# Kernel optimization log

Measured on AMD Instinct MI355X. Metric: run time of the kernel, lower is better.

## Reference

```python
import jax, jax.numpy as jnp
import numpy as np

D_MODEL = 1024
NUM_HEADS = 16
MAX_LEN = 500
D_K = D_MODEL // NUM_HEADS


def setup_inputs() -> dict:
    key = jax.random.key(0)
    ks = jax.random.split(key, 10)
    B, L = 8, 500
    s = 1.0 / np.sqrt(D_MODEL)
    return {
        "query": jax.random.normal(ks[0], (B, L, D_MODEL), dtype=jnp.float32),
        "key": jax.random.normal(ks[1], (B, L, D_MODEL), dtype=jnp.float32),
        "value": jax.random.normal(ks[2], (B, L, D_MODEL), dtype=jnp.float32),
        "Wq": jax.random.normal(ks[3], (D_MODEL, D_MODEL), dtype=jnp.float32) * s,
        "bq": jnp.zeros((D_MODEL,), dtype=jnp.float32),
        "Wk": jax.random.normal(ks[4], (D_MODEL, D_MODEL), dtype=jnp.float32) * s,
        "bk": jnp.zeros((D_MODEL,), dtype=jnp.float32),
        "Wv": jax.random.normal(ks[5], (D_MODEL, D_MODEL), dtype=jnp.float32) * s,
        "bv": jnp.zeros((D_MODEL,), dtype=jnp.float32),
        "rel_emb": jax.random.normal(ks[6], (NUM_HEADS, 2 * MAX_LEN - 1), dtype=jnp.float32),
    }


def reference(query, key, value, Wq, bq, Wk, bk, Wv, bv, rel_emb):
    B, Lq, _ = query.shape
    Lk = key.shape[1]
    H, dk = NUM_HEADS, D_K
    # QKV projections -> [B, H, L, d]
    q = (query @ Wq + bq).reshape(B, Lq, H, dk).transpose(0, 2, 1, 3)
    k = (key @ Wk + bk).reshape(B, Lk, H, dk).transpose(0, 2, 1, 3)
    v = (value @ Wv + bv).reshape(B, Lk, H, dk).transpose(0, 2, 1, 3)
    scores = jnp.einsum('bhqd,bhkd->bhqk', q, k) / jnp.sqrt(jnp.float32(dk))
    # gathered relative-position bias: [H, Lq, Lk]
    rel_idx = jnp.arange(Lq)[:, None] - jnp.arange(Lk)[None, :] + MAX_LEN - 1
    bias = rel_emb[:, rel_idx]  # [H, Lq, Lk]
    scores = scores + bias[None]
    attn = jax.nn.softmax(scores, axis=-1)
    out = jnp.einsum('bhqk,bhkd->bhqd', attn, v)
    return out.transpose(0, 2, 1, 3).reshape(B, Lq, H * dk)
```

## Files before the change

### kernel.cpp

```cpp
#include <hip/hip_runtime.h>

typedef short bf16x8 __attribute__((ext_vector_type(8)));
typedef float f32x4 __attribute__((ext_vector_type(4)));
typedef unsigned uint4v __attribute__((ext_vector_type(4)));

#define B_    8
#define L_    500
#define LP    512
#define H_    16
#define DK    64
#define DM    1024
#define MP    4096
#define NT    8

static __device__ __forceinline__ unsigned short f2bf(float x) {
  unsigned u = __float_as_uint(x);
  u += 0x7fffu + ((u >> 16) & 1u);
  return (unsigned short)(u >> 16);
}

static __device__ __forceinline__ unsigned cvtpk(float lo, float hi) {
  unsigned r;
  asm("v_cvt_pk_bf16_f32 %0, %1, %2" : "=v"(r) : "v"(lo), "v"(hi));
  return r;
}

static __device__ __forceinline__ void gload16(const void* g, void* l) {
  __builtin_amdgcn_global_load_lds(
      (const __attribute__((address_space(1))) void*)g,
      (__attribute__((address_space(3))) void*)l, 16, 0, 0);
}

__global__ __launch_bounds__(256) void conv_x_kernel(
    const float* __restrict__ iq, const float* __restrict__ ik,
    const float* __restrict__ iv, unsigned short* __restrict__ X) {
  const int z = blockIdx.y;
  const float* src = (z == 0) ? iq : (z == 1) ? ik : iv;
  const size_t flat = (size_t)blockIdx.x * 256 + threadIdx.x;
  const size_t off = flat * 8;
  const int m = (int)(off >> 10);
  unsigned short o[8];
  if (m < 4000) {
    const float4 a = *(const float4*)(src + off);
    const float4 b = *(const float4*)(src + off + 4);
    o[0]=f2bf(a.x); o[1]=f2bf(a.y); o[2]=f2bf(a.z); o[3]=f2bf(a.w);
    o[4]=f2bf(b.x); o[5]=f2bf(b.y); o[6]=f2bf(b.z); o[7]=f2bf(b.w);
  } else {
#pragma unroll
    for (int i = 0; i < 8; ++i) o[i] = 0;
  }
  uint4 pk;
  pk.x = (unsigned)o[0] | ((unsigned)o[1] << 16);
  pk.y = (unsigned)o[2] | ((unsigned)o[3] << 16);
  pk.z = (unsigned)o[4] | ((unsigned)o[5] << 16);
  pk.w = (unsigned)o[6] | ((unsigned)o[7] << 16);
  *(uint4*)(X + (size_t)z * MP * DM + off) = pk;
}

__global__ __launch_bounds__(256) void conv_w_kernel(
    const float* __restrict__ wq, const float* __restrict__ wk,
    const float* __restrict__ wv, unsigned short* __restrict__ Wt) {
  const int z = blockIdx.y;
  const float* W = (z == 0) ? wq : (z == 1) ? wk : wv;
  const int k0 = (blockIdx.x >> 4) * 64;
  const int n0 = (blockIdx.x & 15) * 64;
  __shared__ float t[64][65];
  const int tid = threadIdx.x;
  const int row = tid >> 2;
  const int cb  = (tid & 3) * 16;
#pragma unroll
  for (int s = 0; s < 4; ++s) {
    const float4 v = *(const float4*)(W + (size_t)(k0 + row) * DM + n0 + cb + s * 4);
    t[row][cb + s * 4 + 0] = v.x; t[row][cb + s * 4 + 1] = v.y;
    t[row][cb + s * 4 + 2] = v.z; t[row][cb + s * 4 + 3] = v.w;
  }
  __syncthreads();
  const int nr = tid >> 2;
  const int kb = (tid & 3) * 16;
#pragma unroll
  for (int s = 0; s < 2; ++s) {
    unsigned short o[8];
#pragma unroll
    for (int e = 0; e < 8; ++e) o[e] = f2bf(t[kb + s * 8 + e][nr]);
    uint4 pk;
    pk.x = (unsigned)o[0] | ((unsigned)o[1] << 16);
    pk.y = (unsigned)o[2] | ((unsigned)o[3] << 16);
    pk.z = (unsigned)o[4] | ((unsigned)o[5] << 16);
    pk.w = (unsigned)o[6] | ((unsigned)o[7] << 16);
    *(uint4*)(Wt + (size_t)z * DM * DM + (size_t)(n0 + nr) * DM + k0 + kb + s * 8) = pk;
  }
}

__global__ __launch_bounds__(256) void gemm_qkv_kernel(
    const unsigned short* __restrict__ X, const unsigned short* __restrict__ Wt,
    const float* __restrict__ bq, const float* __restrict__ bk,
    const float* __restrict__ bv,
    unsigned short* __restrict__ qo, unsigned short* __restrict__ ko,
    unsigned short* __restrict__ vo) {
  const int z = blockIdx.y;
  const unsigned short* A  = X  + (size_t)z * MP * DM;
  const unsigned short* Bw = Wt + (size_t)z * DM * DM;
  const float* bias = (z == 0) ? bq : (z == 1) ? bk : bv;
  unsigned short* out = (z == 0) ? qo : (z == 1) ? ko : vo;

  const int bid = blockIdx.x;
  const int xg = bid & 7, y = bid >> 3;
  const int tm = xg + 8 * (y >> 3);
  const int tn = y & 7;
  const int tid = threadIdx.x;
  const int lane = tid & 63, wid = tid >> 6;
  const int wr = wid >> 1, wc = wid & 1;
  const int lg = lane >> 4, lr = lane & 15;

  __shared__ unsigned short sA[2][128 * 32];
  __shared__ unsigned short sB[2][128 * 32];

  const int c0 = tid, c1 = tid + 256;
  const int ar0 = c0 >> 2, ak0 = (c0 & 3) * 8;
  const int ar1 = c1 >> 2, ak1 = (c1 & 3) * 8;
  const unsigned short* Ab = A  + (size_t)tm * 128 * DM;
  const unsigned short* Bb = Bw + (size_t)tn * 128 * DM;

  f32x4 acc[4][4];
#pragma unroll
  for (int i = 0; i < 4; ++i)
#pragma unroll
    for (int j = 0; j < 4; ++j) acc[i][j] = (f32x4){0.f, 0.f, 0.f, 0.f};

  gload16(Ab + (size_t)ar0 * DM + ak0, &sA[0][c0 * 8]);
  gload16(Ab + (size_t)ar1 * DM + ak1, &sA[0][c1 * 8]);
  gload16(Bb + (size_t)ar0 * DM + ak0, &sB[0][c0 * 8]);
  gload16(Bb + (size_t)ar1 * DM + ak1, &sB[0][c1 * 8]);
  asm volatile("s_waitcnt vmcnt(0)" ::: "memory");
  __syncthreads();

  int cur = 0;
  for (int t = 0; t < 32; ++t) {
    if (t < 31) {
      const int kn = (t + 1) * 32;
      gload16(Ab + (size_t)ar0 * DM + kn + ak0, &sA[cur ^ 1][c0 * 8]);
      gload16(Ab + (size_t)ar1 * DM + kn + ak1, &sA[cur ^ 1][c1 * 8]);
      gload16(Bb + (size_t)ar0 * DM + kn + ak0, &sB[cur ^ 1][c0 * 8]);
      gload16(Bb + (size_t)ar1 * DM + kn + ak1, &sB[cur ^ 1][c1 * 8]);
    }
    bf16x8 af[4], bfr[4];
#pragma unroll
    for (int s = 0; s < 4; ++s) {
      af[s]  = *(const bf16x8*)&sA[cur][(wr * 64 + s * 16 + lr) * 32 + lg * 8];
      bfr[s] = *(const bf16x8*)&sB[cur][(wc * 64 + s * 16 + lr) * 32 + lg * 8];
    }
#pragma unroll
    for (int i = 0; i < 4; ++i)
#pragma unroll
      for (int j = 0; j < 4; ++j)
        acc[i][j] = __builtin_amdgcn_mfma_f32_16x16x32_bf16(af[i], bfr[j], acc[i][j], 0, 0, 0);
    asm volatile("s_waitcnt vmcnt(0)" ::: "memory");
    __syncthreads();
    cur ^= 1;
  }

  const int nbase = tn * 128 + wc * 64 + lr;
  float bias4[4];
#pragma unroll
  for (int ns = 0; ns < 4; ++ns) bias4[ns] = bias[nbase + ns * 16];

#pragma unroll
  for (int ms = 0; ms < 4; ++ms) {
#pragma unroll
    for (int r = 0; r < 4; ++r) {
      const int m = tm * 128 + wr * 64 + ms * 16 + lg * 4 + r;
      if (m < 4000) {
        const unsigned batch = (unsigned)m / 500u;
        const int lrow = m - (int)batch * 500;
#pragma unroll
        for (int ns = 0; ns < 4; ++ns) {
          const int n = nbase + ns * 16;
          const int hh = n >> 6, d = n & 63;
          out[(((size_t)batch * H_ + hh) * LP + lrow) * DK + d] =
              f2bf(acc[ms][ns][r] + bias4[ns]);
        }
      }
    }
  }
}

__global__ __launch_bounds__(256) void transpose_v_kernel(
    const unsigned short* __restrict__ v, unsigned short* __restrict__ vt) {
  const int bh = blockIdx.y;
  const int l0 = blockIdx.x * 64;
  __shared__ unsigned short t[64][72];
  const int tid = threadIdx.x;
  const int lrw = tid >> 2, dc = (tid & 3) * 16;
  const int gl = l0 + lrw;
  if (gl < L_) {
    *(uint4*)&t[lrw][dc]     = *(const uint4*)(v + ((size_t)bh * LP + gl) * DK + dc);
    *(uint4*)&t[lrw][dc + 8] = *(const uint4*)(v + ((size_t)bh * LP + gl) * DK + dc + 8);
  } else {
    const uint4 zz = {0u, 0u, 0u, 0u};
    *(uint4*)&t[lrw][dc]     = zz;
    *(uint4*)&t[lrw][dc + 8] = zz;
  }
  __syncthreads();
  const int dr = tid >> 2, lcb = (tid & 3) * 16;
#pragma unroll
  for (int s = 0; s < 2; ++s) {
    unsigned short e[8];
#pragma unroll
    for (int i = 0; i < 8; ++i) e[i] = t[lcb + s * 8 + i][dr];
    uint4 o;
    o.x = (unsigned)e[0] | ((unsigned)e[1] << 16);
    o.y = (unsigned)e[2] | ((unsigned)e[3] << 16);
    o.z = (unsigned)e[4] | ((unsigned)e[5] << 16);
    o.w = (unsigned)e[6] | ((unsigned)e[7] << 16);
    *(uint4*)(vt + ((size_t)bh * DK + dr) * LP + l0 + lcb + s * 8) = o;
  }
}

__global__ __launch_bounds__(256, 4) void attn_kernel(
    const unsigned short* __restrict__ q, const unsigned short* __restrict__ k,
    const unsigned short* __restrict__ vt, const float* __restrict__ rel,
    float* __restrict__ out) {
  const int id = blockIdx.x;
  const int bh = id & 127, qc = id >> 7;
  const int b = bh >> 4, h = bh & 15;
  const int tid = threadIdx.x;
  const int lane = tid & 63, wid = tid >> 6;
  const int lg = lane >> 4, lr = lane & 15;

  __shared__ unsigned short kt[2][2][64][32];
  __shared__ unsigned short vtt[2][2][64][32];
  __shared__ float relb[576];

  const float LOG2E = 1.44269504f;
  const float SC = 0.125f * LOG2E;
  const int rbase = qc * 64 - 12;
  for (int i = tid; i < 575; i += 256) {
    int idx = rbase + i;
    idx = idx < 0 ? 0 : (idx > 998 ? 998 : idx);
    relb[i] = rel[h * 999 + idx] * LOG2E;
  }

  const int qrow = qc * 64 + wid * 16 + lr;
  const unsigned short* qp = q + ((size_t)bh * LP + qrow) * DK + lg * 8;
  const bf16x8 qf0 = *(const bf16x8*)qp;
  const bf16x8 qf1 = *(const bf16x8*)(qp + 32);

  const int kj = tid >> 2, dc = (tid & 3) * 16;
  const unsigned short* kgp = k + ((size_t)bh * LP + kj) * DK + dc;
  unsigned short* kls = &kt[0][dc >> 5][kj][dc & 31];
  const int vd = tid >> 2, vkg = (tid & 3) * 16;
  const unsigned short* vgp = vt + ((size_t)bh * DK + vd) * LP + vkg;
  unsigned short* vls = &vtt[0][vkg >> 5][vd][vkg & 31];

  const int sig0 = 8 * (lr >> 2) + (lr & 3);
  const int qin = wid * 16 + lr;

  f32x4 o[4];
#pragma unroll
  for (int d = 0; d < 4; ++d) o[d] = (f32x4){0.f, 0.f, 0.f, 0.f};
  float mrun = -1e30f, lrun = 0.f;

  uint4 ka0 = *(const uint4*)(kgp);
  uint4 ka1 = *(const uint4*)(kgp + 8);
  uint4 va0 = *(const uint4*)(vgp);
  uint4 va1 = *(const uint4*)(vgp + 8);

  for (int t = 0; t < NT; ++t) {
    const int buf = t & 1;
    *(uint4*)(kls + buf * 4096)     = ka0;
    *(uint4*)(kls + buf * 4096 + 8) = ka1;
    *(uint4*)(vls + buf * 4096)     = va0;
    *(uint4*)(vls + buf * 4096 + 8) = va1;
    __syncthreads();

    if (t < NT - 1) {
      const size_t ko_ = (size_t)(t + 1) * 64 * DK;
      ka0 = *(const uint4*)(kgp + ko_);
      ka1 = *(const uint4*)(kgp + ko_ + 8);
      va0 = *(const uint4*)(vgp + (t + 1) * 64);
      va1 = *(const uint4*)(vgp + (t + 1) * 64 + 8);
    }

    f32x4 s[2][2];
#pragma unroll
    for (int kc = 0; kc < 2; ++kc)
#pragma unroll
      for (int hf = 0; hf < 2; ++hf) {
        const int sg = kc * 32 + hf * 4 + sig0;
        const bf16x8 a0 = *(const bf16x8*)&kt[buf][0][sg][lg * 8];
        const bf16x8 a1 = *(const bf16x8*)&kt[buf][1][sg][lg * 8];
        f32x4 ss = (f32x4){0.f, 0.f, 0.f, 0.f};
        ss = __builtin_amdgcn_mfma_f32_16x16x32_bf16(a0, qf0, ss, 0, 0, 0);
        ss = __builtin_amdgcn_mfma_f32_16x16x32_bf16(a1, qf1, ss, 0, 0, 0);
        s[kc][hf] = ss;
      }

    float sc[2][2][4];
#pragma unroll
    for (int kc = 0; kc < 2; ++kc)
#pragma unroll
      for (int hf = 0; hf < 2; ++hf) {
        const int bidx = qin - (t * 64 + kc * 32 + 8 * lg + 4 * hf) + 511;
#pragma unroll
        for (int r = 0; r < 4; ++r)
          sc[kc][hf][r] = s[kc][hf][r] * SC + relb[bidx - r];
      }
    if (t == NT - 1) {
#pragma unroll
      for (int hf = 0; hf < 2; ++hf)
#pragma unroll
        for (int r = 0; r < 4; ++r)
          if (8 * lg + 4 * hf + r >= 20) sc[1][hf][r] = -1e30f;
    }

    float m0 = fmaxf(fmaxf(sc[0][0][0], sc[0][0][1]), fmaxf(sc[0][0][2], sc[0][0][3]));
    float m1 = fmaxf(fmaxf(sc[0][1][0], sc[0][1][1]), fmaxf(sc[0][1][2], sc[0][1][3]));
    float m2 = fmaxf(fmaxf(sc[1][0][0], sc[1][0][1]), fmaxf(sc[1][0][2], sc[1][0][3]));
    float m3 = fmaxf(fmaxf(sc[1][1][0], sc[1][1][1]), fmaxf(sc[1][1][2], sc[1][1][3]));
    const float mloc = fmaxf(fmaxf(m0, m1), fmaxf(m2, m3));
    if (!__all(mloc - mrun <= 11.5f)) {
      float mx = fmaxf(mloc, mrun);
      mx = fmaxf(mx, __shfl_xor(mx, 16));
      mx = fmaxf(mx, __shfl_xor(mx, 32));
      const float alpha = exp2f(mrun - mx);
      mrun = mx;
      lrun *= alpha;
#pragma unroll
      for (int d = 0; d < 4; ++d) {
        o[d][0] *= alpha; o[d][1] *= alpha; o[d][2] *= alpha; o[d][3] *= alpha;
      }
    }

    float rs = 0.f;
    unsigned pw[2][4];
#pragma unroll
    for (int kc = 0; kc < 2; ++kc)
#pragma unroll
      for (int hf = 0; hf < 2; ++hf) {
        float p0 = exp2f(sc[kc][hf][0] - mrun);
        float p1 = exp2f(sc[kc][hf][1] - mrun);
        float p2 = exp2f(sc[kc][hf][2] - mrun);
        float p3 = exp2f(sc[kc][hf][3] - mrun);
        rs += (p0 + p1) + (p2 + p3);
        pw[kc][hf * 2 + 0] = cvtpk(p0, p1);
        pw[kc][hf * 2 + 1] = cvtpk(p2, p3);
      }
    rs += __shfl_xor(rs, 16);
    rs += __shfl_xor(rs, 32);
    lrun += rs;

#pragma unroll
    for (int kc = 0; kc < 2; ++kc) {
      union { uint4v u; bf16x8 v; } cv;
      cv.u = (uint4v){pw[kc][0], pw[kc][1], pw[kc][2], pw[kc][3]};
      const bf16x8 pf = cv.v;
#pragma unroll
      for (int db = 0; db < 4; ++db) {
        const bf16x8 vf = *(const bf16x8*)&vtt[buf][kc][db * 16 + lr][lg * 8];
        o[db] = __builtin_amdgcn_mfma_f32_16x16x32_bf16(vf, pf, o[db], 0, 0, 0);
      }
    }
  }

  if (qrow < L_) {
    const float inv = 1.0f / lrun;
    float* op = out + ((size_t)b * L_ + qrow) * DM + h * DK + lg * 4;
#pragma unroll
    for (int db = 0; db < 4; ++db) {
      float4 v;
      v.x = o[db][0] * inv; v.y = o[db][1] * inv;
      v.z = o[db][2] * inv; v.w = o[db][3] * inv;
      *(float4*)(op + db * 16) = v;
    }
  }
}

extern "C" void kernel_launch(void* const* d_in, const int* in_sizes, int n_in,
                              void* d_out, int out_size, void* d_ws, size_t ws_size,
                              hipStream_t stream) {
  const float* iq  = (const float*)d_in[0];
  const float* ik  = (const float*)d_in[1];
  const float* iv  = (const float*)d_in[2];
  const float* wq  = (const float*)d_in[3];
  const float* bq  = (const float*)d_in[4];
  const float* wk  = (const float*)d_in[5];
  const float* bk  = (const float*)d_in[6];
  const float* wv  = (const float*)d_in[7];
  const float* bv  = (const float*)d_in[8];
  const float* rel = (const float*)d_in[9];
  float* out = (float*)d_out;

  char* w = (char*)d_ws;
  unsigned short* X   = (unsigned short*)(w);
  unsigned short* Wt  = (unsigned short*)(w + 25165824);
  unsigned short* qb  = (unsigned short*)(w + 31457280);
  unsigned short* kb  = (unsigned short*)(w + 39845888);
  unsigned short* vb  = (unsigned short*)(w + 48234496);
  unsigned short* vtb = (unsigned short*)(w);

  conv_x_kernel<<<dim3(2048, 3), 256, 0, stream>>>(iq, ik, iv, X);
  conv_w_kernel<<<dim3(256, 3), 256, 0, stream>>>(wq, wk, wv, Wt);
  gemm_qkv_kernel<<<dim3(256, 3), 256, 0, stream>>>(X, Wt, bq, bk, bv, qb, kb, vb);
  transpose_v_kernel<<<dim3(8, 128), 256, 0, stream>>>(vb, vtb);
  attn_kernel<<<1024, 256, 0, stream>>>(qb, kb, vtb, rel, out);
}
```

Measured before the change: 90.91 us.

## Restructure QKV GEMM into 256x256 tiles with ping-pong pipelined MFMA schedule

The QKV projection GEMM moves from 128x128 tiles with 256 threads and BK=32 to 256x256 tiles with 512 threads (8 waves) and BK=64. LDS uses an XOR swizzle, and staging is split into quarter-steps interleaved with MFMA clusters under s_setprio and barriers. Block-to-XCD mapping is remapped for L2 locality. The aim is higher arithmetic intensity and better overlap of loads with MFMA, at the cost of only 192 blocks on a 256-CU GPU, which leaves many CUs idle, plus heavy register and LDS use.

After: 85.16 us. 1.07x faster.

```diff
diff --git a/kernel.cpp b/kernel.cpp
--- a/kernel.cpp
+++ b/kernel.cpp
@@ -29,6 +29,10 @@
   __builtin_amdgcn_global_load_lds(
       (const __attribute__((address_space(1))) void*)g,
       (__attribute__((address_space(3))) void*)l, 16, 0, 0);
+}
+
+static __device__ __forceinline__ f32x4 MF(bf16x8 a, bf16x8 b, f32x4 c) {
+  return __builtin_amdgcn_mfma_f32_16x16x32_bf16(a, b, c, 0, 0, 0);
 }
 
 __global__ __launch_bounds__(256) void conv_x_kernel(
@@ -91,93 +95,148 @@
   }
 }
 
-__global__ __launch_bounds__(256) void gemm_qkv_kernel(
+#define BAR()   __builtin_amdgcn_s_barrier()
+#define LGKM0() do { asm volatile("s_waitcnt lgkmcnt(0)" ::: "memory"); \
+                     __builtin_amdgcn_sched_barrier(0); } while (0)
+#define VM0()   asm volatile("s_waitcnt vmcnt(0)" ::: "memory")
+#define PRIO1() __builtin_amdgcn_s_setprio(1)
+#define PRIO0() __builtin_amdgcn_s_setprio(0)
+
+#define HALF_STEP(BK_, KTS_, DOST_)                                              \
+  {                                                                              \
+                      \
+    _Pragma("unroll") for (int mi = 0; mi < 4; ++mi) {                           \
+      aF[mi][0] = rdA(BK_, mi, 0); aF[mi][1] = rdA(BK_, mi, 1); }                \
+    _Pragma("unroll") for (int ni = 0; ni < 2; ++ni) {                           \
+      bF[ni][0] = rdB(BK_, ni, 0); bF[ni][1] = rdB(BK_, ni, 1); }                \
+    if (DOST_) { STAGE((&sA[1 - (BK_)][0][0]), GA0, KTS_);                       \
+                 STAGE((&sA[1 - (BK_)][1][0]), GA1, KTS_); }                     \
+    BAR(); LGKM0(); PRIO1();                                                     \
+    _Pragma("unroll") for (int mi = 0; mi < 4; ++mi)                             \
+      _Pragma("unroll") for (int ni = 0; ni < 2; ++ni) {                         \
+        acc[mi][ni] = MF(aF[mi][0], bF[ni][0], acc[mi][ni]);                     \
+        acc[mi][ni] = MF(aF[mi][1], bF[ni][1], acc[mi][ni]); }                   \
+    PRIO0(); BAR();                                                              \
+                                            \
+    _Pragma("unroll") for (int ni = 0; ni < 2; ++ni) {                           \
+      bF2[ni][0] = rdB(BK_, 2 + ni, 0); bF2[ni][1] = rdB(BK_, 2 + ni, 1); }      \
+    if (DOST_) { STAGE((&sB[1 - (BK_)][0][0]), GB0, KTS_); }                     \
+    BAR(); LGKM0(); PRIO1();                                                     \
+    _Pragma("unroll") for (int mi = 0; mi < 4; ++mi)                             \
+      _Pragma("unroll") for (int ni = 0; ni < 2; ++ni) {                         \
+        acc[mi][2 + ni] = MF(aF[mi][0], bF2[ni][0], acc[mi][2 + ni]);            \
+        acc[mi][2 + ni] = MF(aF[mi][1], bF2[ni][1], acc[mi][2 + ni]); }          \
+    PRIO0(); BAR();                                                              \
+                                            \
+    _Pragma("unroll") for (int mi = 0; mi < 4; ++mi) {                           \
+      aF[mi][0] = rdA(BK_, 4 + mi, 0); aF[mi][1] = rdA(BK_, 4 + mi, 1); }        \
+    if (DOST_) { STAGE((&sB[1 - (BK_)][1][0]), GB1, KTS_); }                     \
+    BAR(); LGKM0(); PRIO1();                                                     \
+    _Pragma("unroll") for (int mi = 0; mi < 4; ++mi)                             \
+      _Pragma("unroll") for (int ni = 0; ni < 2; ++ni) {                         \
+        acc[4 + mi][2 + ni] = MF(aF[mi][0], bF2[ni][0], acc[4 + mi][2 + ni]);    \
+        acc[4 + mi][2 + ni] = MF(aF[mi][1], bF2[ni][1], acc[4 + mi][2 + ni]); }  \
+    PRIO0(); BAR();                                                              \
+                 \
+    _Pragma("unroll") for (int ni = 0; ni < 2; ++ni) {                           \
+      bF[ni][0] = rdB(BK_, ni, 0); bF[ni][1] = rdB(BK_, ni, 1); }                \
+    VM0();                                                                       \
+    BAR(); LGKM0(); PRIO1();                                                     \
+    _Pragma("unroll") for (int mi = 0; mi < 4; ++mi)                             \
+      _Pragma("unroll") for (int ni = 0; ni < 2; ++ni) {                         \
+        acc[4 + mi][ni] = MF(aF[mi][0], bF[ni][0], acc[4 + mi][ni]);             \
+        acc[4 + mi][ni] = MF(aF[mi][1], bF[ni][1], acc[4 + mi][ni]); }           \
+    PRIO0(); BAR();                                                              \
+  }
+
+__global__ __launch_bounds__(512, 2) void gemm_qkv_kernel(
     const unsigned short* __restrict__ X, const unsigned short* __restrict__ Wt,
     const float* __restrict__ bq, const float* __restrict__ bk,
     const float* __restrict__ bv,
     unsigned short* __restrict__ qo, unsigned short* __restrict__ ko,
     unsigned short* __restrict__ vo) {
-  const int z = blockIdx.y;
+  const int bid = blockIdx.x;
+  const int z = bid >> 6, r = bid & 63;
+  const int xcd = r & 7, j = r >> 3;
+  const int tm = (xcd & 3) * 4 + (j & 3);
+  const int tn = (xcd >> 2) * 2 + (j >> 2);
   const unsigned short* A  = X  + (size_t)z * MP * DM;
   const unsigned short* Bw = Wt + (size_t)z * DM * DM;
   const float* bias = (z == 0) ? bq : (z == 1) ? bk : bv;
   unsigned short* out = (z == 0) ? qo : (z == 1) ? ko : vo;
 
-  const int bid = blockIdx.x;
-  const int xg = bid & 7, y = bid >> 3;
-  const int tm = xg + 8 * (y >> 3);
-  const int tn = y & 7;
   const int tid = threadIdx.x;
   const int lane = tid & 63, wid = tid >> 6;
-  const int wr = wid >> 1, wc = wid & 1;
+  const int wr = wid >> 2, wcol = wid & 3;
   const int lg = lane >> 4, lr = lane & 15;
 
-  __shared__ unsigned short sA[2][128 * 32];
-  __shared__ unsigned short sB[2][128 * 32];
-
-  const int c0 = tid, c1 = tid + 256;
-  const int ar0 = c0 >> 2, ak0 = (c0 & 3) * 8;
-  const int ar1 = c1 >> 2, ak1 = (c1 & 3) * 8;
-  const unsigned short* Ab = A  + (size_t)tm * 128 * DM;
-  const unsigned short* Bb = Bw + (size_t)tn * 128 * DM;
-
-  f32x4 acc[4][4];
-#pragma unroll
-  for (int i = 0; i < 4; ++i)
-#pragma unroll
-    for (int j = 0; j < 4; ++j) acc[i][j] = (f32x4){0.f, 0.f, 0.f, 0.f};
-
-  gload16(Ab + (size_t)ar0 * DM + ak0, &sA[0][c0 * 8]);
-  gload16(Ab + (size_t)ar1 * DM + ak1, &sA[0][c1 * 8]);
-  gload16(Bb + (size_t)ar0 * DM + ak0, &sB[0][c0 * 8]);
-  gload16(Bb + (size_t)ar1 * DM + ak1, &sB[0][c1 * 8]);
-  asm volatile("s_waitcnt vmcnt(0)" ::: "memory");
-  __syncthreads();
-
-  int cur = 0;
-  for (int t = 0; t < 32; ++t) {
-    if (t < 31) {
-      const int kn = (t + 1) * 32;
-      gload16(Ab + (size_t)ar0 * DM + kn + ak0, &sA[cur ^ 1][c0 * 8]);
-      gload16(Ab + (size_t)ar1 * DM + kn + ak1, &sA[cur ^ 1][c1 * 8]);
-      gload16(Bb + (size_t)ar0 * DM + kn + ak0, &sB[cur ^ 1][c0 * 8]);
-      gload16(Bb + (size_t)ar1 * DM + kn + ak1, &sB[cur ^ 1][c1 * 8]);
-    }
-    bf16x8 af[4], bfr[4];
-#pragma unroll
-    for (int s = 0; s < 4; ++s) {
-      af[s]  = *(const bf16x8*)&sA[cur][(wr * 64 + s * 16 + lr) * 32 + lg * 8];
-      bfr[s] = *(const bf16x8*)&sB[cur][(wc * 64 + s * 16 + lr) * 32 + lg * 8];
-    }
-#pragma unroll
-    for (int i = 0; i < 4; ++i)
-#pragma unroll
-      for (int j = 0; j < 4; ++j)
-        acc[i][j] = __builtin_amdgcn_mfma_f32_16x16x32_bf16(af[i], bfr[j], acc[i][j], 0, 0, 0);
-    asm volatile("s_waitcnt vmcnt(0)" ::: "memory");
-    __syncthreads();
-    cur ^= 1;
-  }
-
-  const int nbase = tn * 128 + wc * 64 + lr;
+  __shared__ __attribute__((aligned(16))) unsigned short sA[2][2][128 * 64];
+  __shared__ __attribute__((aligned(16))) unsigned short sB[2][2][128 * 64];
+
+  const int ch0 = tid, ch1 = tid + 512;
+  const int row0 = ch0 >> 3, row1 = ch1 >> 3;
+  const size_t so0 = (size_t)row0 * DM + (size_t)(((ch0 & 7) ^ (row0 & 7)) * 8);
+  const size_t so1 = (size_t)row1 * DM + (size_t)(((ch1 & 7) ^ (row1 & 7)) * 8);
+  const int lo0 = ch0 * 8, lo1 = ch1 * 8;
+  const unsigned short* GA0 = A  + (size_t)(tm * 256) * DM;
+  const unsigned short* GA1 = GA0 + (size_t)128 * DM;
+  const unsigned short* GB0 = Bw + (size_t)(tn * 256) * DM;
+  const unsigned short* GB1 = GB0 + (size_t)128 * DM;
+
+  auto STAGE = [&](unsigned short* L, const unsigned short* G, int kt) {
+    gload16(G + so0 + kt * 64, L + lo0);
+    gload16(G + so1 + kt * 64, L + lo1);
+  };
+
+  const int swzb = (lr & 7) << 4;
+  auto rdA = [&](int bk_, int mi, int kk) {
+    const int ush = (mi * 16 + lr) * 64 + (((kk * 64 + lg * 16) ^ swzb) >> 1);
+    return *(const bf16x8*)&sA[bk_][wr][ush];
+  };
+  auto rdB = [&](int bk_, int ni, int kk) {
+    const int ush = ((wcol & 1) * 64 + ni * 16 + lr) * 64 +
+                    (((kk * 64 + lg * 16) ^ swzb) >> 1);
+    return *(const bf16x8*)&sB[bk_][wcol >> 1][ush];
+  };
+
+  f32x4 acc[8][4];
+#pragma unroll
+  for (int i = 0; i < 8; ++i)
+#pragma unroll
+    for (int jj = 0; jj < 4; ++jj) acc[i][jj] = (f32x4){0.f, 0.f, 0.f, 0.f};
+
+  STAGE(&sA[0][0][0], GA0, 0);
+  STAGE(&sA[0][1][0], GA1, 0);
+  STAGE(&sB[0][0][0], GB0, 0);
+  STAGE(&sB[0][1][0], GB1, 0);
+  VM0();
+  BAR();
+
+  bf16x8 aF[4][2], bF[2][2], bF2[2][2];
+  for (int i = 0; i < 8; ++i) {
+    HALF_STEP(0, 2 * i + 1, true);
+    HALF_STEP(1, 2 * i + 2, (i < 7));
+  }
+
+  const int nb = tn * 256 + wcol * 64 + lr;
   float bias4[4];
 #pragma unroll
-  for (int ns = 0; ns < 4; ++ns) bias4[ns] = bias[nbase + ns * 16];
-
-#pragma unroll
-  for (int ms = 0; ms < 4; ++ms) {
-#pragma unroll
-    for (int r = 0; r < 4; ++r) {
-      const int m = tm * 128 + wr * 64 + ms * 16 + lg * 4 + r;
+  for (int ni = 0; ni < 4; ++ni) bias4[ni] = bias[nb + ni * 16];
+
+#pragma unroll
+  for (int mi = 0; mi < 8; ++mi) {
+#pragma unroll
+    for (int rr = 0; rr < 4; ++rr) {
+      const int m = tm * 256 + wr * 128 + mi * 16 + lg * 4 + rr;
       if (m < 4000) {
         const unsigned batch = (unsigned)m / 500u;
         const int lrow = m - (int)batch * 500;
 #pragma unroll
-        for (int ns = 0; ns < 4; ++ns) {
-          const int n = nbase + ns * 16;
+        for (int ni = 0; ni < 4; ++ni) {
+          const int n = nb + ni * 16;
           const int hh = n >> 6, d = n & 63;
           out[(((size_t)batch * H_ + hh) * LP + lrow) * DK + d] =
-              f2bf(acc[ms][ns][r] + bias4[ns]);
+              f2bf(acc[mi][ni][rr] + bias4[ni]);
         }
       }
     }
@@ -400,7 +459,7 @@
 
   conv_x_kernel<<<dim3(2048, 3), 256, 0, stream>>>(iq, ik, iv, X);
   conv_w_kernel<<<dim3(256, 3), 256, 0, stream>>>(wq, wk, wv, Wt);
-  gemm_qkv_kernel<<<dim3(256, 3), 256, 0, stream>>>(X, Wt, bq, bk, bv, qb, kb, vb);
+  gemm_qkv_kernel<<<192, 512, 0, stream>>>(X, Wt, bq, bk, bv, qb, kb, vb);
   transpose_v_kernel<<<dim3(8, 128), 256, 0, stream>>>(vb, vtb);
   attn_kernel<<<1024, 256, 0, stream>>>(qb, kb, vtb, rel, out);
 }
```

## Restructure QKV GEMM with 256x64 tiles, 4-stage LDS pipeline and XCD-aware mapping

Applied to the files above, without the earlier changes.

The QKV projection GEMM moves from 128x128 double-buffered tiles to 256x64 tiles with a 4-deep LDS ring, using partial vmcnt waits so three stages of loads stay in flight. Blocks are remapped from a 1D grid so each XCD works on a contiguous patch of M/N tiles for L2 locality, and the MFMA section runs at raised wave priority. The aim is to hide global-load latency and improve cache reuse. In exchange it uses more LDS per block (80KB), which may limit occupancy despite the launch-bounds hint of 2, and the narrower N tile reloads A more often.

Result: slower. 102.9 us (+13.2%).

```diff
diff --git a/kernel.cpp b/kernel.cpp
--- a/kernel.cpp
+++ b/kernel.cpp
@@ -29,6 +29,10 @@
   __builtin_amdgcn_global_load_lds(
       (const __attribute__((address_space(1))) void*)g,
       (__attribute__((address_space(3))) void*)l, 16, 0, 0);
+}
+
+static __device__ __forceinline__ f32x4 MF(bf16x8 a, bf16x8 b, f32x4 c) {
+  return __builtin_amdgcn_mfma_f32_16x16x32_bf16(a, b, c, 0, 0, 0);
 }
 
 __global__ __launch_bounds__(256) void conv_x_kernel(
@@ -91,35 +95,42 @@
   }
 }
 
-__global__ __launch_bounds__(256) void gemm_qkv_kernel(
+__global__ __launch_bounds__(256, 2) void gemm_qkv_kernel(
     const unsigned short* __restrict__ X, const unsigned short* __restrict__ Wt,
     const float* __restrict__ bq, const float* __restrict__ bk,
     const float* __restrict__ bv,
     unsigned short* __restrict__ qo, unsigned short* __restrict__ ko,
     unsigned short* __restrict__ vo) {
-  const int z = blockIdx.y;
+  const int bid = blockIdx.x;
+  const int xcd = bid & 7, idx = bid >> 3;
+  const int z = idx >> 5, r = idx & 31;
+  const int tm = (xcd & 3) * 4 + (r & 3);
+  const int tn = (xcd >> 2) * 8 + (r >> 2);
   const unsigned short* A  = X  + (size_t)z * MP * DM;
   const unsigned short* Bw = Wt + (size_t)z * DM * DM;
   const float* bias = (z == 0) ? bq : (z == 1) ? bk : bv;
   unsigned short* out = (z == 0) ? qo : (z == 1) ? ko : vo;
 
-  const int bid = blockIdx.x;
-  const int xg = bid & 7, y = bid >> 3;
-  const int tm = xg + 8 * (y >> 3);
-  const int tn = y & 7;
   const int tid = threadIdx.x;
   const int lane = tid & 63, wid = tid >> 6;
-  const int wr = wid >> 1, wc = wid & 1;
   const int lg = lane >> 4, lr = lane & 15;
 
-  __shared__ unsigned short sA[2][128 * 32];
-  __shared__ unsigned short sB[2][128 * 32];
-
-  const int c0 = tid, c1 = tid + 256;
-  const int ar0 = c0 >> 2, ak0 = (c0 & 3) * 8;
-  const int ar1 = c1 >> 2, ak1 = (c1 & 3) * 8;
-  const unsigned short* Ab = A  + (size_t)tm * 128 * DM;
-  const unsigned short* Bb = Bw + (size_t)tn * 128 * DM;
+  __shared__ __attribute__((aligned(16))) unsigned short sA[4][256 * 32];
+  __shared__ __attribute__((aligned(16))) unsigned short sB[4][64 * 32];
+
+  const unsigned short* GA = A  + (size_t)(tm * 256) * DM;
+  const unsigned short* GB = Bw + (size_t)(tn * 64) * DM;
+
+  auto STAGE = [&](int t) {
+    const int buf = t & 3;
+    const int kof = t * 32;
+#pragma unroll
+    for (int j = 0; j < 4; ++j) {
+      const int c = j * 256 + tid;
+      gload16(GA + (size_t)(c >> 2) * DM + kof + (c & 3) * 8, &sA[buf][c * 8]);
+    }
+    gload16(GB + (size_t)(tid >> 2) * DM + kof + (tid & 3) * 8, &sB[buf][tid * 8]);
+  };
 
   f32x4 acc[4][4];
 #pragma unroll
@@ -127,58 +138,63 @@
 #pragma unroll
     for (int j = 0; j < 4; ++j) acc[i][j] = (f32x4){0.f, 0.f, 0.f, 0.f};
 
-  gload16(Ab + (size_t)ar0 * DM + ak0, &sA[0][c0 * 8]);
-  gload16(Ab + (size_t)ar1 * DM + ak1, &sA[0][c1 * 8]);
-  gload16(Bb + (size_t)ar0 * DM + ak0, &sB[0][c0 * 8]);
-  gload16(Bb + (size_t)ar1 * DM + ak1, &sB[0][c1 * 8]);
+  auto COMPUTE = [&](int t) {
+    const int buf = t & 3;
+    bf16x8 aF[4], bF[4];
+#pragma unroll
+    for (int mi = 0; mi < 4; ++mi)
+      aF[mi] = *(const bf16x8*)&sA[buf][(wid * 64 + mi * 16 + lr) * 32 + lg * 8];
+#pragma unroll
+    for (int ni = 0; ni < 4; ++ni)
+      bF[ni] = *(const bf16x8*)&sB[buf][(ni * 16 + lr) * 32 + lg * 8];
+    __builtin_amdgcn_s_setprio(1);
+#pragma unroll
+    for (int mi = 0; mi < 4; ++mi)
+#pragma unroll
+      for (int ni = 0; ni < 4; ++ni)
+        acc[mi][ni] = MF(aF[mi], bF[ni], acc[mi][ni]);
+    __builtin_amdgcn_s_setprio(0);
+  };
+
+  STAGE(0); STAGE(1); STAGE(2);
+  asm volatile("s_waitcnt vmcnt(10)" ::: "memory");
+  __builtin_amdgcn_s_barrier();
+  __builtin_amdgcn_sched_barrier(0);
+
+  for (int t = 0; t < 29; ++t) {
+    STAGE(t + 3);
+    COMPUTE(t);
+    asm volatile("s_waitcnt vmcnt(10)" ::: "memory");
+    __builtin_amdgcn_s_barrier();
+    __builtin_amdgcn_sched_barrier(0);
+  }
+  COMPUTE(29);
+  asm volatile("s_waitcnt vmcnt(5)" ::: "memory");
+  __builtin_amdgcn_s_barrier();
+  __builtin_amdgcn_sched_barrier(0);
+  COMPUTE(30);
   asm volatile("s_waitcnt vmcnt(0)" ::: "memory");
-  __syncthreads();
-
-  int cur = 0;
-  for (int t = 0; t < 32; ++t) {
-    if (t < 31) {
-      const int kn = (t + 1) * 32;
-      gload16(Ab + (size_t)ar0 * DM + kn + ak0, &sA[cur ^ 1][c0 * 8]);
-      gload16(Ab + (size_t)ar1 * DM + kn + ak1, &sA[cur ^ 1][c1 * 8]);
-      gload16(Bb + (size_t)ar0 * DM + kn + ak0, &sB[cur ^ 1][c0 * 8]);
-      gload16(Bb + (size_t)ar1 * DM + kn + ak1, &sB[cur ^ 1][c1 * 8]);
-    }
-    bf16x8 af[4], bfr[4];
-#pragma unroll
-    for (int s = 0; s < 4; ++s) {
-      af[s]  = *(const bf16x8*)&sA[cur][(wr * 64 + s * 16 + lr) * 32 + lg * 8];
-      bfr[s] = *(const bf16x8*)&sB[cur][(wc * 64 + s * 16 + lr) * 32 + lg * 8];
-    }
-#pragma unroll
-    for (int i = 0; i < 4; ++i)
-#pragma unroll
-      for (int j = 0; j < 4; ++j)
-        acc[i][j] = __builtin_amdgcn_mfma_f32_16x16x32_bf16(af[i], bfr[j], acc[i][j], 0, 0, 0);
-    asm volatile("s_waitcnt vmcnt(0)" ::: "memory");
-    __syncthreads();
-    cur ^= 1;
-  }
-
-  const int nbase = tn * 128 + wc * 64 + lr;
+  __builtin_amdgcn_s_barrier();
+  __builtin_amdgcn_sched_barrier(0);
+  COMPUTE(31);
+
   float bias4[4];
 #pragma unroll
-  for (int ns = 0; ns < 4; ++ns) bias4[ns] = bias[nbase + ns * 16];
-
-#pragma unroll
-  for (int ms = 0; ms < 4; ++ms) {
-#pragma unroll
-    for (int r = 0; r < 4; ++r) {
-      const int m = tm * 128 + wr * 64 + ms * 16 + lg * 4 + r;
+  for (int ni = 0; ni < 4; ++ni) bias4[ni] = bias[tn * 64 + ni * 16 + lr];
+
+#pragma unroll
+  for (int mi = 0; mi < 4; ++mi) {
+#pragma unroll
+    for (int rr = 0; rr < 4; ++rr) {
+      const int m = tm * 256 + wid * 64 + mi * 16 + lg * 4 + rr;
       if (m < 4000) {
         const unsigned batch = (unsigned)m / 500u;
         const int lrow = m - (int)batch * 500;
-#pragma unroll
-        for (int ns = 0; ns < 4; ++ns) {
-          const int n = nbase + ns * 16;
-          const int hh = n >> 6, d = n & 63;
-          out[(((size_t)batch * H_ + hh) * LP + lrow) * DK + d] =
-              f2bf(acc[ms][ns][r] + bias4[ns]);
-        }
+        unsigned short* op =
+            out + (((size_t)batch * H_ + tn) * LP + lrow) * DK + lr;
+#pragma unroll
+        for (int ni = 0; ni < 4; ++ni)
+          op[ni * 16] = f2bf(acc[mi][ni][rr] + bias4[ni]);
       }
     }
   }
@@ -400,7 +416,7 @@
 
   conv_x_kernel<<<dim3(2048, 3), 256, 0, stream>>>(iq, ik, iv, X);
   conv_w_kernel<<<dim3(256, 3), 256, 0, stream>>>(wq, wk, wv, Wt);
-  gemm_qkv_kernel<<<dim3(256, 3), 256, 0, stream>>>(X, Wt, bq, bk, bv, qb, kb, vb);
+  gemm_qkv_kernel<<<768, 256, 0, stream>>>(X, Wt, bq, bk, bv, qb, kb, vb);
   transpose_v_kernel<<<dim3(8, 128), 256, 0, stream>>>(vb, vtb);
   attn_kernel<<<1024, 256, 0, stream>>>(qb, kb, vtb, rel, out);
 }
```

## Fuse fp32-to-bf16 activation conversion into QKV GEMM and swizzle LDS tiles

Applied to the files above, without the earlier changes.

Removes the separate conversion kernel for query/key/value. The GEMM now loads fp32 activations into registers, converts them to bf16 with packed convert instructions, and writes them to LDS after the MFMA loop, so the loads for the next tile overlap compute. It also adds an XOR swizzle to the A and B LDS layouts to reduce bank conflicts. This avoids writing and re-reading a 24MB bf16 staging buffer and one kernel launch. In exchange the GEMM reads twice the activation bytes and carries more register pressure.

Result: slower. 223.8 us (+146.2%).

```diff
diff --git a/kernel.cpp b/kernel.cpp
--- a/kernel.cpp
+++ b/kernel.cpp
@@ -10,7 +10,6 @@
 #define H_    16
 #define DK    64
 #define DM    1024
-#define MP    4096
 #define NT    8
 
 static __device__ __forceinline__ unsigned short f2bf(float x) {
@@ -31,30 +30,8 @@
       (__attribute__((address_space(3))) void*)l, 16, 0, 0);
 }
 
-__global__ __launch_bounds__(256) void conv_x_kernel(
-    const float* __restrict__ iq, const float* __restrict__ ik,
-    const float* __restrict__ iv, unsigned short* __restrict__ X) {
-  const int z = blockIdx.y;
-  const float* src = (z == 0) ? iq : (z == 1) ? ik : iv;
-  const size_t flat = (size_t)blockIdx.x * 256 + threadIdx.x;
-  const size_t off = flat * 8;
-  const int m = (int)(off >> 10);
-  unsigned short o[8];
-  if (m < 4000) {
-    const float4 a = *(const float4*)(src + off);
-    const float4 b = *(const float4*)(src + off + 4);
-    o[0]=f2bf(a.x); o[1]=f2bf(a.y); o[2]=f2bf(a.z); o[3]=f2bf(a.w);
-    o[4]=f2bf(b.x); o[5]=f2bf(b.y); o[6]=f2bf(b.z); o[7]=f2bf(b.w);
-  } else {
-#pragma unroll
-    for (int i = 0; i < 8; ++i) o[i] = 0;
-  }
-  uint4 pk;
-  pk.x = (unsigned)o[0] | ((unsigned)o[1] << 16);
-  pk.y = (unsigned)o[2] | ((unsigned)o[3] << 16);
-  pk.z = (unsigned)o[4] | ((unsigned)o[5] << 16);
-  pk.w = (unsigned)o[6] | ((unsigned)o[7] << 16);
-  *(uint4*)(X + (size_t)z * MP * DM + off) = pk;
+static __device__ __forceinline__ f32x4 MF(bf16x8 a, bf16x8 b, f32x4 c) {
+  return __builtin_amdgcn_mfma_f32_16x16x32_bf16(a, b, c, 0, 0, 0);
 }
 
 __global__ __launch_bounds__(256) void conv_w_kernel(
@@ -92,13 +69,14 @@
 }
 
 __global__ __launch_bounds__(256) void gemm_qkv_kernel(
-    const unsigned short* __restrict__ X, const unsigned short* __restrict__ Wt,
+    const float* __restrict__ xq, const float* __restrict__ xk,
+    const float* __restrict__ xv, const unsigned short* __restrict__ Wt,
     const float* __restrict__ bq, const float* __restrict__ bk,
     const float* __restrict__ bv,
     unsigned short* __restrict__ qo, unsigned short* __restrict__ ko,
     unsigned short* __restrict__ vo) {
   const int z = blockIdx.y;
-  const unsigned short* A  = X  + (size_t)z * MP * DM;
+  const float* Af = (z == 0) ? xq : (z == 1) ? xk : xv;
   const unsigned short* Bw = Wt + (size_t)z * DM * DM;
   const float* bias = (z == 0) ? bq : (z == 1) ? bk : bv;
   unsigned short* out = (z == 0) ? qo : (z == 1) ? ko : vo;
@@ -112,14 +90,48 @@
   const int wr = wid >> 1, wc = wid & 1;
   const int lg = lane >> 4, lr = lane & 15;
 
-  __shared__ unsigned short sA[2][128 * 32];
-  __shared__ unsigned short sB[2][128 * 32];
+  __shared__ __attribute__((aligned(16))) unsigned short sA[2][128 * 32];
+  __shared__ __attribute__((aligned(16))) unsigned short sB[2][128 * 32];
 
   const int c0 = tid, c1 = tid + 256;
-  const int ar0 = c0 >> 2, ak0 = (c0 & 3) * 8;
-  const int ar1 = c1 >> 2, ak1 = (c1 & 3) * 8;
-  const unsigned short* Ab = A  + (size_t)tm * 128 * DM;
+  const int ar0 = c0 >> 2, ag0 = c0 & 3;
+  const int ar1 = c1 >> 2, ag1 = c1 & 3;
+  const int m0 = tm * 128 + ar0, m1 = tm * 128 + ar1;
+  const bool ok0 = m0 < 4000, ok1 = m1 < 4000;
+  const float* pA0 = Af + (size_t)m0 * DM + ag0 * 8;
+  const float* pA1 = Af + (size_t)m1 * DM + ag1 * 8;
+  const int aw0 = ar0 * 32 + ((ag0 ^ (ar0 & 3)) * 8);
+  const int aw1 = ar1 * 32 + ((ag1 ^ (ar1 & 3)) * 8);
   const unsigned short* Bb = Bw + (size_t)tn * 128 * DM;
+  const size_t bs0 = (size_t)ar0 * DM + (size_t)((ag0 ^ (ar0 & 3)) * 8);
+  const size_t bs1 = (size_t)ar1 * DM + (size_t)((ag1 ^ (ar1 & 3)) * 8);
+
+  float4 ra0, ra1, ra2, ra3;
+  const float4 fz = {0.f, 0.f, 0.f, 0.f};
+
+  auto LOADA = [&](int t) {
+    if (ok0) {
+      ra0 = *(const float4*)(pA0 + t * 32);
+      ra1 = *(const float4*)(pA0 + t * 32 + 4);
+    } else { ra0 = fz; ra1 = fz; }
+    if (ok1) {
+      ra2 = *(const float4*)(pA1 + t * 32);
+      ra3 = *(const float4*)(pA1 + t * 32 + 4);
+    } else { ra2 = fz; ra3 = fz; }
+  };
+  auto STAGEB = [&](int t, int buf) {
+    gload16(Bb + bs0 + t * 32, &sB[buf][c0 * 8]);
+    gload16(Bb + bs1 + t * 32, &sB[buf][c1 * 8]);
+  };
+  auto WRITEA = [&](int buf) {
+    uint4 w0, w1;
+    w0.x = cvtpk(ra0.x, ra0.y); w0.y = cvtpk(ra0.z, ra0.w);
+    w0.z = cvtpk(ra1.x, ra1.y); w0.w = cvtpk(ra1.z, ra1.w);
+    w1.x = cvtpk(ra2.x, ra2.y); w1.y = cvtpk(ra2.z, ra2.w);
+    w1.z = cvtpk(ra3.x, ra3.y); w1.w = cvtpk(ra3.z, ra3.w);
+    *(uint4*)&sA[buf][aw0] = w0;
+    *(uint4*)&sA[buf][aw1] = w1;
+  };
 
   f32x4 acc[4][4];
 #pragma unroll
@@ -127,34 +139,31 @@
 #pragma unroll
     for (int j = 0; j < 4; ++j) acc[i][j] = (f32x4){0.f, 0.f, 0.f, 0.f};
 
-  gload16(Ab + (size_t)ar0 * DM + ak0, &sA[0][c0 * 8]);
-  gload16(Ab + (size_t)ar1 * DM + ak1, &sA[0][c1 * 8]);
-  gload16(Bb + (size_t)ar0 * DM + ak0, &sB[0][c0 * 8]);
-  gload16(Bb + (size_t)ar1 * DM + ak1, &sB[0][c1 * 8]);
-  asm volatile("s_waitcnt vmcnt(0)" ::: "memory");
+  LOADA(0);
+  STAGEB(0, 0);
+  WRITEA(0);
   __syncthreads();
 
+  const int swz = (lr & 3);
   int cur = 0;
   for (int t = 0; t < 32; ++t) {
     if (t < 31) {
-      const int kn = (t + 1) * 32;
-      gload16(Ab + (size_t)ar0 * DM + kn + ak0, &sA[cur ^ 1][c0 * 8]);
-      gload16(Ab + (size_t)ar1 * DM + kn + ak1, &sA[cur ^ 1][c1 * 8]);
-      gload16(Bb + (size_t)ar0 * DM + kn + ak0, &sB[cur ^ 1][c0 * 8]);
-      gload16(Bb + (size_t)ar1 * DM + kn + ak1, &sB[cur ^ 1][c1 * 8]);
+      LOADA(t + 1);
+      STAGEB(t + 1, cur ^ 1);
+      __builtin_amdgcn_sched_barrier(0);
     }
     bf16x8 af[4], bfr[4];
 #pragma unroll
     for (int s = 0; s < 4; ++s) {
-      af[s]  = *(const bf16x8*)&sA[cur][(wr * 64 + s * 16 + lr) * 32 + lg * 8];
-      bfr[s] = *(const bf16x8*)&sB[cur][(wc * 64 + s * 16 + lr) * 32 + lg * 8];
+      af[s]  = *(const bf16x8*)&sA[cur][(wr * 64 + s * 16 + lr) * 32 + ((lg ^ swz) * 8)];
+      bfr[s] = *(const bf16x8*)&sB[cur][(wc * 64 + s * 16 + lr) * 32 + ((lg ^ swz) * 8)];
     }
 #pragma unroll
     for (int i = 0; i < 4; ++i)
 #pragma unroll
       for (int j = 0; j < 4; ++j)
-        acc[i][j] = __builtin_amdgcn_mfma_f32_16x16x32_bf16(af[i], bfr[j], acc[i][j], 0, 0, 0);
-    asm volatile("s_waitcnt vmcnt(0)" ::: "memory");
+        acc[i][j] = MF(af[i], bfr[j], acc[i][j]);
+    if (t < 31) WRITEA(cur ^ 1);
     __syncthreads();
     cur ^= 1;
   }
@@ -391,16 +400,14 @@
   float* out = (float*)d_out;
 
   char* w = (char*)d_ws;
-  unsigned short* X   = (unsigned short*)(w);
   unsigned short* Wt  = (unsigned short*)(w + 25165824);
   unsigned short* qb  = (unsigned short*)(w + 31457280);
   unsigned short* kb  = (unsigned short*)(w + 39845888);
   unsigned short* vb  = (unsigned short*)(w + 48234496);
   unsigned short* vtb = (unsigned short*)(w);
 
-  conv_x_kernel<<<dim3(2048, 3), 256, 0, stream>>>(iq, ik, iv, X);
   conv_w_kernel<<<dim3(256, 3), 256, 0, stream>>>(wq, wk, wv, Wt);
-  gemm_qkv_kernel<<<dim3(256, 3), 256, 0, stream>>>(X, Wt, bq, bk, bv, qb, kb, vb);
+  gemm_qkv_kernel<<<dim3(256, 3), 256, 0, stream>>>(iq, ik, iv, Wt, bq, bk, bv, qb, kb, vb);
   transpose_v_kernel<<<dim3(8, 128), 256, 0, stream>>>(vb, vtb);
   attn_kernel<<<1024, 256, 0, stream>>>(qb, kb, vtb, rel, out);
 }
```
